# Performance work log

Hardware: AMD Instinct MI355X
Metric: run time of the kernel (lower is better)

## Reference

```python
import jax, jax.numpy as jnp
import numpy as np

NUM_KERNELS = 301
GAMMA = 10.0
SHIFT = float(np.log(2.0))


def shifted_softplus(x):
    return jax.nn.softplus(x) - SHIFT


def setup_inputs() -> dict:
    key = jax.random.key(0)
    k1, k2, k3, k4, k5, k6 = jax.random.split(key, 6)
    N, F, K = 768, 128, NUM_KERNELS
    x = jax.random.normal(k1, (N, F), dtype=jnp.float32)
    # positions scaled to span a realistic distance range vs centers in [0, 30]
    r = jax.random.uniform(k2, (N, 3), dtype=jnp.float32) * 10.0
    W1 = jax.random.normal(k3, (K, F), dtype=jnp.float32) * (1.0 / np.sqrt(K))
    b1 = jax.random.normal(k4, (F,), dtype=jnp.float32) * 0.01
    W2 = jax.random.normal(k5, (F, F), dtype=jnp.float32) * (1.0 / np.sqrt(F))
    b2 = jax.random.normal(k6, (F,), dtype=jnp.float32) * 0.01
    return {"x": x, "r": r, "W1": W1, "b1": b1, "W2": W2, "b2": b2}


def reference(x, r, W1, b1, W2, b2):
    # pairwise Euclidean distances, safe at the zero diagonal
    diff = r[:, None, :] - r[None, :, :]            # [N, N, 3]
    sq = jnp.sum(diff * diff, axis=-1)              # [N, N]
    d = jnp.where(sq > 0, jnp.sqrt(jnp.where(sq > 0, sq, 1.0)), 0.0)
    centers = jnp.linspace(0.0, 30.0, NUM_KERNELS, dtype=jnp.float32)  # [K]
    expanded = jnp.exp(-GAMMA * jnp.square(d[..., None] - centers))    # [N, N, K]
    h = shifted_softplus(expanded @ W1 + b1)        # [N, N, F]
    w = shifted_softplus(h @ W2 + b2)               # [N, N, F]
    o = jnp.einsum('jk,ijk->ik', x, w)              # [N, F]
    return o
```

## Files before the change

kernel.cpp:

```cpp
#include <hip/hip_runtime.h>

#define F        128
#define NN       768
#define KE       192
#define E_STRIDE 56
#define H_STRIDE 136
#define NT       48
#define NPAIR    (NT*(NT+1)/2)
#define NBLK     (NPAIR*4)

#define L2E 1.44269504f
#define LN2 0.69314718f

typedef __attribute__((ext_vector_type(8))) short short8;
typedef __attribute__((ext_vector_type(4))) float floatx4;

__device__ __forceinline__ unsigned short f2bf(float f) {
    union { float f; unsigned u; } v; v.f = f;
    return (unsigned short)((v.u + 0x8000u) >> 16);
}

__device__ __forceinline__ unsigned cvt_pk_bf16(float lo, float hi) {
    unsigned r;
    asm("v_cvt_pk_bf16_f32 %0, %1, %2" : "=v"(r) : "v"(lo), "v"(hi));
    return r;
}

__device__ __forceinline__ float ssp_l2(float zl2e) {
    float t = exp2f(zl2e);
    float u = __log2f(1.0f + t);
    return fmaf(LN2, u, -LN2);
}

__device__ __forceinline__ void pin(short8& v) { asm volatile("" : "+v"(v)); }

__device__ __forceinline__ void bar_lds() {
    asm volatile("s_waitcnt lgkmcnt(0)" ::: "memory");
    __builtin_amdgcn_s_barrier();
}

__device__ __forceinline__ int klo_from_d(float d) {
    int k = (int)ceilf(fmaf(10.0f, d, -13.0f));
    k &= ~1;
    return k < 0 ? 0 : (k > KE - 32 ? KE - 32 : k);
}

__global__ void prep_w(const float* __restrict__ W1, const float* __restrict__ W2,
                       unsigned short* __restrict__ W1s, unsigned short* __restrict__ W2s,
                       float* __restrict__ out) {
    int idx = blockIdx.x * 256 + threadIdx.x;
    out[idx] = 0.0f;
    if (idx < KE * F) {
        int t = idx & 7, lane = (idx >> 3) & 63, frag = idx >> 9;
        int k = (frag >> 3) * 32 + (lane >> 4) * 8 + t;
        int n = (frag & 7) * 16 + (lane & 15);
        W1s[idx] = f2bf(W1[k * F + n] * L2E);
    } else if (idx < KE * F + F * F) {
        int j = idx - KE * F;
        int t = j & 7, lane = (j >> 3) & 63, frag = j >> 9;
        int k = (frag >> 3) * 32 + (lane >> 4) * 8 + t;
        int n = (frag & 7) * 16 + (lane & 15);
        W2s[j] = f2bf(W2[k * F + n] * L2E);
    }
}

__global__ __launch_bounds__(256, 2) void cfconv_main(
    const float* __restrict__ x, const float* __restrict__ r,
    const float* __restrict__ b1, const float* __restrict__ b2,
    const unsigned short* __restrict__ W1s, const unsigned short* __restrict__ W2s,
    float* __restrict__ out)
{
    __shared__ __align__(16) unsigned short e_lds[64 * E_STRIDE];
    __shared__ __align__(16) unsigned short h_lds[64 * H_STRIDE];
    __shared__ float d_all[64];
    __shared__ unsigned short klo8_lds[64];

    const int tid  = threadIdx.x;
    const int lane = tid & 63;
    const int wave = tid >> 6;
    const int quad = lane >> 4;
    const int l15  = lane & 15;

    int bidx = blockIdx.x;
    const int s = bidx & 3;
    int b = bidx >> 2;
    int A = (int)((97.0f - sqrtf(9409.0f - 8.0f * (float)b)) * 0.5f);
    while ((A + 1) * (97 - (A + 1)) / 2 <= b) ++A;
    while (A * (97 - A) / 2 > b) --A;
    const int B = A + (b - A * (97 - A) / 2);
    const int Ai0 = A * 16, Bj0 = B * 16;
    const bool diag = (A == B);

    short8 w1f[6][2], w2f[4][2];
    #pragma unroll
    for (int ks = 0; ks < KE / 32; ++ks) {
        w1f[ks][0] = *(const short8*)&W1s[((ks*8 + wave*2 + 0) * 64 + lane) * 8];
        w1f[ks][1] = *(const short8*)&W1s[((ks*8 + wave*2 + 1) * 64 + lane) * 8];
    }
    #pragma unroll
    for (int ks = 0; ks < F / 32; ++ks) {
        w2f[ks][0] = *(const short8*)&W2s[((ks*8 + wave*2 + 0) * 64 + lane) * 8];
        w2f[ks][1] = *(const short8*)&W2s[((ks*8 + wave*2 + 1) * 64 + lane) * 8];
    }
    #pragma unroll
    for (int ks = 0; ks < 6; ++ks) { pin(w1f[ks][0]); pin(w1f[ks][1]); }
    #pragma unroll
    for (int ks = 0; ks < 4; ++ks) { pin(w2f[ks][0]); pin(w2f[ks][1]); }

    if (tid < 64) {
        int gi = Ai0 + s * 4 + (tid >> 4), gj = Bj0 + (tid & 15);
        float dx = r[gi*3+0] - r[gj*3+0];
        float dy = r[gi*3+1] - r[gj*3+1];
        float dz = r[gi*3+2] - r[gj*3+2];
        float sq = dx*dx + dy*dy + dz*dz;
        d_all[tid] = sq > 0.0f ? sqrtf(sq) : 0.0f;
    }

    const int c0 = wave * 32 + l15;
    const int c1 = c0 + 16;
    const float b1L0 = b1[c0] * L2E, b1L1 = b1[c1] * L2E;
    const float b2L0 = b2[c0] * L2E, b2L1 = b2[c1] * L2E;

    float xA0[4], xA1[4];
    #pragma unroll
    for (int mt = 0; mt < 4; ++mt) {
        int gi = Ai0 + s*4 + mt;
        xA0[mt] = x[gi * F + c0];
        xA1[mt] = x[gi * F + c1];
    }
    float xB0[4], xB1[4];
    #pragma unroll
    for (int rg = 0; rg < 4; ++rg) {
        int gj = Bj0 + quad * 4 + rg;
        xB0[rg] = x[gj * F + c0];
        xB1[rg] = x[gj * F + c1];
    }

    const int rq16 = 16 * ((l15 >> 2) & 3);

    bar_lds();

    {
        int row = tid >> 2;
        int lo4 = tid & 3;
        float d = d_all[row];
        int klo8 = klo_from_d(d) & ~7;
        if (lo4 == 0) klo8_lds[row] = (unsigned short)klo8;
        unsigned* e32 = (unsigned*)&e_lds[row * E_STRIDE];
        #pragma unroll
        for (int pass = 0; pass < 6; ++pass) {
            int loc = lo4 * 2 + pass * 8;
            float t0 = fmaf(-0.1f, (float)(klo8 + loc), d);
            float t1 = fmaf(-0.1f, (float)(klo8 + loc + 1), d);
            float e0 = exp2f(t0 * t0 * (-10.0f * L2E));
            float e1 = exp2f(t1 * t1 * (-10.0f * L2E));
            e32[loc >> 1] = cvt_pk_bf16(e0, e1);
        }
    }
    bar_lds();

    floatx4 acc[4][2];
    {
        floatx4 bi0 = {b1L0, b1L0, b1L0, b1L0};
        floatx4 bi1 = {b1L1, b1L1, b1L1, b1L1};
        #pragma unroll
        for (int mt = 0; mt < 4; ++mt) { acc[mt][0] = bi0; acc[mt][1] = bi1; }
    }
    int klo8r[4];
    #pragma unroll
    for (int mt = 0; mt < 4; ++mt) klo8r[mt] = klo8_lds[mt*16 + l15];
    __builtin_amdgcn_s_setprio(1);
    #pragma unroll
    for (int ks = 0; ks < KE / 32; ++ks) {
        short8 af[4];
        #pragma unroll
        for (int mt = 0; mt < 4; ++mt) {
            int off = ks*32 + quad*8 - klo8r[mt];
            off = ((unsigned)off > 32u) ? 40 : off;
            af[mt] = *(const short8*)&e_lds[(mt*16 + l15) * E_STRIDE + off];
        }
        #pragma unroll
        for (int mt = 0; mt < 4; ++mt) {
            acc[mt][0] = __builtin_amdgcn_mfma_f32_16x16x32_bf16(af[mt], w1f[ks][0], acc[mt][0], 0, 0, 0);
            acc[mt][1] = __builtin_amdgcn_mfma_f32_16x16x32_bf16(af[mt], w1f[ks][1], acc[mt][1], 0, 0, 0);
        }
    }
    __builtin_amdgcn_s_setprio(0);

    #pragma unroll
    for (int mt = 0; mt < 4; ++mt) {
        #pragma unroll
        for (int rg = 0; rg < 4; ++rg) {
            int row = mt*16 + quad*4 + rg;
            float h0 = ssp_l2(acc[mt][0][rg]);
            float h1 = ssp_l2(acc[mt][1][rg]);
            unsigned pk = cvt_pk_bf16(h0, h1);
            h_lds[row * H_STRIDE + ((c0 + 16*quad) & 127)] = (unsigned short)pk;
            h_lds[row * H_STRIDE + ((c1 + 16*quad) & 127)] = (unsigned short)(pk >> 16);
        }
    }
    bar_lds();

    floatx4 acc2[4][2];
    {
        floatx4 bi0 = {b2L0, b2L0, b2L0, b2L0};
        floatx4 bi1 = {b2L1, b2L1, b2L1, b2L1};
        #pragma unroll
        for (int mt = 0; mt < 4; ++mt) { acc2[mt][0] = bi0; acc2[mt][1] = bi1; }
    }
    __builtin_amdgcn_s_setprio(1);
    #pragma unroll
    for (int ks = 0; ks < F / 32; ++ks) {
        int ko = (ks*32 + quad*8 + rq16) & 127;
        short8 af[4];
        #pragma unroll
        for (int mt = 0; mt < 4; ++mt)
            af[mt] = *(const short8*)&h_lds[(mt*16 + l15) * H_STRIDE + ko];
        #pragma unroll
        for (int mt = 0; mt < 4; ++mt) {
            acc2[mt][0] = __builtin_amdgcn_mfma_f32_16x16x32_bf16(af[mt], w2f[ks][0], acc2[mt][0], 0, 0, 0);
            acc2[mt][1] = __builtin_amdgcn_mfma_f32_16x16x32_bf16(af[mt], w2f[ks][1], acc2[mt][1], 0, 0, 0);
        }
    }
    __builtin_amdgcn_s_setprio(0);

    float oA0[4] = {0,0,0,0}, oA1[4] = {0,0,0,0};
    float oB0[4] = {0,0,0,0}, oB1[4] = {0,0,0,0};
    #pragma unroll
    for (int mt = 0; mt < 4; ++mt) {
        #pragma unroll
        for (int rg = 0; rg < 4; ++rg) {
            float w0 = ssp_l2(acc2[mt][0][rg]);
            float w1 = ssp_l2(acc2[mt][1][rg]);
            oA0[mt] = fmaf(xB0[rg], w0, oA0[mt]);
            oA1[mt] = fmaf(xB1[rg], w1, oA1[mt]);
            if (!diag) {
                oB0[rg] = fmaf(xA0[mt], w0, oB0[rg]);
                oB1[rg] = fmaf(xA1[mt], w1, oB1[rg]);
            }
        }
    }
    #pragma unroll
    for (int mt = 0; mt < 4; ++mt) {
        oA0[mt] += __shfl_xor(oA0[mt], 16, 64); oA0[mt] += __shfl_xor(oA0[mt], 32, 64);
        oA1[mt] += __shfl_xor(oA1[mt], 16, 64); oA1[mt] += __shfl_xor(oA1[mt], 32, 64);
    }
    if (lane < 16) {
        #pragma unroll
        for (int mt = 0; mt < 4; ++mt) {
            int gi = Ai0 + s*4 + mt;
            atomicAdd(&out[gi * F + c0], oA0[mt]);
            atomicAdd(&out[gi * F + c1], oA1[mt]);
        }
    }
    if (!diag) {
        #pragma unroll
        for (int rg = 0; rg < 4; ++rg) {
            int gj = Bj0 + quad * 4 + rg;
            atomicAdd(&out[gj * F + c0], oB0[rg]);
            atomicAdd(&out[gj * F + c1], oB1[rg]);
        }
    }
}

extern "C" void kernel_launch(void* const* d_in, const int* in_sizes, int n_in,
                              void* d_out, int out_size, void* d_ws, size_t ws_size,
                              hipStream_t stream) {
    const float* x  = (const float*)d_in[0];
    const float* r  = (const float*)d_in[1];
    const float* W1 = (const float*)d_in[2];
    const float* b1 = (const float*)d_in[3];
    const float* W2 = (const float*)d_in[4];
    const float* b2 = (const float*)d_in[5];
    float* out = (float*)d_out;

    unsigned short* W1s = (unsigned short*)d_ws;
    unsigned short* W2s = W1s + KE * F;

    prep_w<<<(NN * F) / 256, 256, 0, stream>>>(W1, W2, W1s, W2s, out);
    cfconv_main<<<NBLK, 256, 0, stream>>>(x, r, b1, b2, W1s, W2s, out);
}
```

Measured before the change: 119.3 us.

## Stream weight fragments from global per k-step instead of pinning in registers

Weight fragments for both GEMMs are no longer preloaded and pinned in registers at kernel start. Each k-step now loads them from global/L2, which cuts register pressure and may let more waves run per CU, at the cost of extra memory latency inside the MFMA loops. The Gaussian expansion computes five passes and zero-fills the last slot instead of computing a sixth. The prep kernel now reads W coalesced with a scattered write and zeroes the output with vector stores.

After: 117.9 us, median of 2. No clear change (-1.2%).

```diff
diff --git a/kernel.cpp b/kernel.cpp
--- a/kernel.cpp
+++ b/kernel.cpp
@@ -32,8 +32,6 @@
     return fmaf(LN2, u, -LN2);
 }
 
-__device__ __forceinline__ void pin(short8& v) { asm volatile("" : "+v"(v)); }
-
 __device__ __forceinline__ void bar_lds() {
     asm volatile("s_waitcnt lgkmcnt(0)" ::: "memory");
     __builtin_amdgcn_s_barrier();
@@ -49,18 +47,21 @@
                        unsigned short* __restrict__ W1s, unsigned short* __restrict__ W2s,
                        float* __restrict__ out) {
     int idx = blockIdx.x * 256 + threadIdx.x;
-    out[idx] = 0.0f;
+    if (idx < (NN * F) / 4) {
+        floatx4 z = {0.f, 0.f, 0.f, 0.f};
+        ((floatx4*)out)[idx] = z;
+    }
     if (idx < KE * F) {
-        int t = idx & 7, lane = (idx >> 3) & 63, frag = idx >> 9;
-        int k = (frag >> 3) * 32 + (lane >> 4) * 8 + t;
-        int n = (frag & 7) * 16 + (lane & 15);
-        W1s[idx] = f2bf(W1[k * F + n] * L2E);
+        int k = idx >> 7, n = idx & 127;
+        int frag = (k >> 5) * 8 + (n >> 4);
+        int dst = (frag * 64 + ((k >> 3) & 3) * 16 + (n & 15)) * 8 + (k & 7);
+        W1s[dst] = f2bf(W1[idx] * L2E);
     } else if (idx < KE * F + F * F) {
         int j = idx - KE * F;
-        int t = j & 7, lane = (j >> 3) & 63, frag = j >> 9;
-        int k = (frag >> 3) * 32 + (lane >> 4) * 8 + t;
-        int n = (frag & 7) * 16 + (lane & 15);
-        W2s[j] = f2bf(W2[k * F + n] * L2E);
+        int k = j >> 7, n = j & 127;
+        int frag = (k >> 5) * 8 + (n >> 4);
+        int dst = (frag * 64 + ((k >> 3) & 3) * 16 + (n & 15)) * 8 + (k & 7);
+        W2s[dst] = f2bf(W2[j] * L2E);
     }
 }
 
@@ -91,22 +92,6 @@
     const int Ai0 = A * 16, Bj0 = B * 16;
     const bool diag = (A == B);
 
-    short8 w1f[6][2], w2f[4][2];
-    #pragma unroll
-    for (int ks = 0; ks < KE / 32; ++ks) {
-        w1f[ks][0] = *(const short8*)&W1s[((ks*8 + wave*2 + 0) * 64 + lane) * 8];
-        w1f[ks][1] = *(const short8*)&W1s[((ks*8 + wave*2 + 1) * 64 + lane) * 8];
-    }
-    #pragma unroll
-    for (int ks = 0; ks < F / 32; ++ks) {
-        w2f[ks][0] = *(const short8*)&W2s[((ks*8 + wave*2 + 0) * 64 + lane) * 8];
-        w2f[ks][1] = *(const short8*)&W2s[((ks*8 + wave*2 + 1) * 64 + lane) * 8];
-    }
-    #pragma unroll
-    for (int ks = 0; ks < 6; ++ks) { pin(w1f[ks][0]); pin(w1f[ks][1]); }
-    #pragma unroll
-    for (int ks = 0; ks < 4; ++ks) { pin(w2f[ks][0]); pin(w2f[ks][1]); }
-
     if (tid < 64) {
         int gi = Ai0 + s * 4 + (tid >> 4), gj = Bj0 + (tid & 15);
         float dx = r[gi*3+0] - r[gj*3+0];
@@ -137,6 +122,8 @@
     }
 
     const int rq16 = 16 * ((l15 >> 2) & 3);
+    const unsigned short* w1base = W1s + (wave * 2 * 64 + lane) * 8;
+    const unsigned short* w2base = W2s + (wave * 2 * 64 + lane) * 8;
 
     bar_lds();
 
@@ -148,7 +135,7 @@
         if (lo4 == 0) klo8_lds[row] = (unsigned short)klo8;
         unsigned* e32 = (unsigned*)&e_lds[row * E_STRIDE];
         #pragma unroll
-        for (int pass = 0; pass < 6; ++pass) {
+        for (int pass = 0; pass < 5; ++pass) {
             int loc = lo4 * 2 + pass * 8;
             float t0 = fmaf(-0.1f, (float)(klo8 + loc), d);
             float t1 = fmaf(-0.1f, (float)(klo8 + loc + 1), d);
@@ -156,6 +143,7 @@
             float e1 = exp2f(t1 * t1 * (-10.0f * L2E));
             e32[loc >> 1] = cvt_pk_bf16(e0, e1);
         }
+        e32[20 + lo4] = 0u;
     }
     bar_lds();
 
@@ -172,6 +160,8 @@
     __builtin_amdgcn_s_setprio(1);
     #pragma unroll
     for (int ks = 0; ks < KE / 32; ++ks) {
+        short8 w0 = *(const short8*)&w1base[(ks*8 + 0) * 512];
+        short8 w1 = *(const short8*)&w1base[(ks*8 + 1) * 512];
         short8 af[4];
         #pragma unroll
         for (int mt = 0; mt < 4; ++mt) {
@@ -181,8 +171,8 @@
         }
         #pragma unroll
         for (int mt = 0; mt < 4; ++mt) {
-            acc[mt][0] = __builtin_amdgcn_mfma_f32_16x16x32_bf16(af[mt], w1f[ks][0], acc[mt][0], 0, 0, 0);
-            acc[mt][1] = __builtin_amdgcn_mfma_f32_16x16x32_bf16(af[mt], w1f[ks][1], acc[mt][1], 0, 0, 0);
+            acc[mt][0] = __builtin_amdgcn_mfma_f32_16x16x32_bf16(af[mt], w0, acc[mt][0], 0, 0, 0);
+            acc[mt][1] = __builtin_amdgcn_mfma_f32_16x16x32_bf16(af[mt], w1, acc[mt][1], 0, 0, 0);
         }
     }
     __builtin_amdgcn_s_setprio(0);
@@ -211,6 +201,8 @@
     __builtin_amdgcn_s_setprio(1);
     #pragma unroll
     for (int ks = 0; ks < F / 32; ++ks) {
+        short8 w0 = *(const short8*)&w2base[(ks*8 + 0) * 512];
+        short8 w1 = *(const short8*)&w2base[(ks*8 + 1) * 512];
         int ko = (ks*32 + quad*8 + rq16) & 127;
         short8 af[4];
         #pragma unroll
@@ -218,8 +210,8 @@
             af[mt] = *(const short8*)&h_lds[(mt*16 + l15) * H_STRIDE + ko];
         #pragma unroll
         for (int mt = 0; mt < 4; ++mt) {
-            acc2[mt][0] = __builtin_amdgcn_mfma_f32_16x16x32_bf16(af[mt], w2f[ks][0], acc2[mt][0], 0, 0, 0);
-            acc2[mt][1] = __builtin_amdgcn_mfma_f32_16x16x32_bf16(af[mt], w2f[ks][1], acc2[mt][1], 0, 0, 0);
+            acc2[mt][0] = __builtin_amdgcn_mfma_f32_16x16x32_bf16(af[mt], w0, acc2[mt][0], 0, 0, 0);
+            acc2[mt][1] = __builtin_amdgcn_mfma_f32_16x16x32_bf16(af[mt], w1, acc2[mt][1], 0, 0, 0);
         }
     }
     __builtin_amdgcn_s_setprio(0);
```
